# Kernel optimization log

Hardware: AMD Instinct MI355X
Metric: run time of the kernel (lower is better)

The kernel has to match this reference:

```python
import jax, jax.numpy as jnp
import numpy as np

N_NODES = 100000
N_EDGES = 1600000
D_IN = 128
D_HID = 128
LATENT = 64
N_GRAPHS = 512


def setup_inputs() -> dict:
    key = jax.random.key(0)
    ks = jax.random.split(key, 10)
    x = jax.random.normal(ks[0], (N_NODES, D_IN), dtype=jnp.float32)
    edge_index = jax.random.randint(ks[1], (2, N_EDGES), 0, N_NODES, dtype=jnp.int64)
    batch = jnp.sort(jax.random.randint(ks[2], (N_NODES,), 0, N_GRAPHS, dtype=jnp.int64))
    def lin(k, fan_in, fan_out):
        return jax.random.normal(k, (fan_in, fan_out), dtype=jnp.float32) / np.sqrt(fan_in)
    W1 = lin(ks[3], D_IN, D_HID); b1 = jnp.zeros((D_HID,), jnp.float32)
    W2 = lin(ks[4], D_HID, D_HID); b2 = jnp.zeros((D_HID,), jnp.float32)
    W3 = lin(ks[5], D_HID, 2 * LATENT); b3 = jnp.zeros((2 * LATENT,), jnp.float32)
    return {"x": x, "edge_index": edge_index, "batch": batch,
            "W1": W1, "b1": b1, "W2": W2, "b2": b2, "W3": W3, "b3": b3}


def _gcn_norm(edge_index, n_nodes):
    # PyG GCNConv default: add self-loops, symmetric normalization
    loop = jnp.arange(n_nodes, dtype=edge_index.dtype)
    src = jnp.concatenate([edge_index[0], loop])
    dst = jnp.concatenate([edge_index[1], loop])
    deg = jax.ops.segment_sum(jnp.ones_like(dst, dtype=jnp.float32), dst,
                              num_segments=n_nodes)
    dinv = jnp.where(deg > 0, jax.lax.rsqrt(deg), 0.0)
    norm = dinv[src] * dinv[dst]  # [E + N]
    return src, dst, norm


def _gcn_conv(x, W, b, src, dst, norm, n_nodes):
    h = x @ W                               # [N, d_out]
    msg = h[src] * norm[:, None]            # gather + scale, [E+N, d_out]
    agg = jax.ops.segment_sum(msg, dst, num_segments=n_nodes)
    return agg + b


def reference(x, edge_index, batch, W1, b1, W2, b2, W3, b3):
    n = x.shape[0]
    src, dst, norm = _gcn_norm(edge_index, n)
    h = jax.nn.relu(_gcn_conv(x, W1, b1, src, dst, norm, n))
    h = jax.nn.relu(_gcn_conv(h, W2, b2, src, dst, norm, n))
    h = _gcn_conv(h, W3, b3, src, dst, norm, n)
    # scatter_mean over batch ids -> [num_graphs, 2*latent]
    cnt = jax.ops.segment_sum(jnp.ones((n,), jnp.float32), batch,
                              num_segments=N_GRAPHS)
    summed = jax.ops.segment_sum(h, batch, num_segments=N_GRAPHS)
    return summed / jnp.maximum(cnt, 1.0)[:, None]
```

## Files before the change

kernel.cpp:

```cpp
#include <hip/hip_runtime.h>
#include <stdint.h>

typedef unsigned short u16;
typedef unsigned int   u32;

#define N_NODES  100000
#define N_EDGES  1600000
#define DFEAT    128
#define N_GRAPHS 512

#define NBKT   391
#define EPB    8192
#define NBLK_E 196
#define LBUF   8192

typedef float f32x4 __attribute__((ext_vector_type(4)));
typedef short s16x8 __attribute__((ext_vector_type(8)));

__device__ __forceinline__ float bflo(u32 u) { return __uint_as_float(u << 16); }
__device__ __forceinline__ float bfhi(u32 u) { return __uint_as_float(u & 0xffff0000u); }
__device__ __forceinline__ u16 f2bf(float f) {
  u32 u = __float_as_uint(f);
  return (u16)((u + 0x7fffu + ((u >> 16) & 1u)) >> 16);
}
__device__ __forceinline__ u32 pack2(float f0, float f1) {
  return (u32)f2bf(f0) | ((u32)f2bf(f1) << 16);
}

__device__ __forceinline__ int ld_src(const int* ei, int m, int e) {
  return m ? ei[2 * e] : ei[e];
}
__device__ __forceinline__ int ld_dst(const int* ei, int m, int e) {
  return m ? ei[2 * (N_EDGES + e)] : ei[N_EDGES + e];
}

__device__ __forceinline__ int detect_m_block(const int* __restrict__ ei, int* sm) {
  int t = threadIdx.x;
  if (t < 64) {
    int v = ei[2 * t + 1];
    unsigned long long b = __ballot(v != 0);
    if (t == 0) *sm = (b == 0ull) ? 1 : 0;
  }
  __syncthreads();
  return *sm;
}

__global__ __launch_bounds__(256) void histA_k(const int* __restrict__ ei,
                                               int* __restrict__ ghist,
                                               const float* __restrict__ W1,
                                               const float* __restrict__ W2,
                                               const float* __restrict__ W3,
                                               u16* __restrict__ T1, u16* __restrict__ T2,
                                               u16* __restrict__ T3, int* __restrict__ flag) {
  int t = threadIdx.x, b = blockIdx.x;
  if (b >= NBLK_E) {
    int r = b - NBLK_E;
    if (r < 3) {
      const float* W = (r == 0) ? W1 : (r == 1) ? W2 : W3;
      u16* T         = (r == 0) ? T1 : (r == 1) ? T2 : T3;
      for (int i = t; i < DFEAT * DFEAT; i += 256) {
        int n = i >> 7, k = i & 127;
        T[i] = f2bf(W[k * DFEAT + n]);
      }
    } else {
      if (t < 64) {
        int v = ei[2 * t + 1];
        unsigned long long mm = __ballot(v != 0);
        if (t == 0) *flag = (mm == 0ull) ? 1 : 0;
      }
    }
    return;
  }
  __shared__ int sm;
  __shared__ int hist[NBKT];
  int m = detect_m_block(ei, &sm);
  for (int i = t; i < NBKT; i += 256) hist[i] = 0;
  __syncthreads();
  int e0 = b * EPB;
#pragma unroll
  for (int p = 0; p < EPB / 256; p++) {
    int e = e0 + p * 256 + t;
    if (e < N_EDGES) atomicAdd(&hist[ld_dst(ei, m, e) >> 8], 1);
  }
  __syncthreads();
  for (int i = t; i < NBKT; i += 256) ghist[b * NBKT + i] = hist[i];
}

__global__ __launch_bounds__(256) void scanB1_k(int* __restrict__ ghist,
                                                int* __restrict__ gtot) {
  __shared__ int ts[256];
  int t = threadIdx.x, k = blockIdx.x;
  int v = (t < NBLK_E) ? ghist[t * NBKT + k] : 0;
  ts[t] = v;
  for (int off = 1; off < 256; off <<= 1) {
    __syncthreads(); int add = (t >= off) ? ts[t - off] : 0;
    __syncthreads(); ts[t] += add;
  }
  __syncthreads();
  if (t < NBLK_E) ghist[t * NBKT + k] = ts[t] - v;
  if (t == 255) gtot[k] = ts[255];
}

__device__ __forceinline__ void scan_gtot_block(const int* __restrict__ gtot,
                                                int* bb, int* sc) {
  int t = threadIdx.x;
  int v0 = gtot[t];
  sc[t] = v0;
  for (int off = 1; off < 256; off <<= 1) {
    __syncthreads(); int add = (t >= off) ? sc[t - off] : 0;
    __syncthreads(); sc[t] += add;
  }
  __syncthreads();
  bb[t] = sc[t] - v0;
  int base256 = sc[255];
  __syncthreads();
  int v1 = (t < NBKT - 256) ? gtot[256 + t] : 0;
  sc[t] = v1;
  for (int off = 1; off < 256; off <<= 1) {
    __syncthreads(); int add = (t >= off) ? sc[t - off] : 0;
    __syncthreads(); sc[t] += add;
  }
  __syncthreads();
  if (t < NBKT - 256) bb[256 + t] = base256 + sc[t] - v1;
  if (t == 0) bb[NBKT] = N_EDGES;
  __syncthreads();
}

__global__ __launch_bounds__(256) void scatterC_k(const int* __restrict__ ei,
                                                  const int* __restrict__ obase,
                                                  const int* __restrict__ gtot,
                                                  u32* __restrict__ colpk) {
  __shared__ int sm;
  __shared__ int cur[NBKT];
  __shared__ int bb[NBKT + 1];
  __shared__ int sc[256];
  int t = threadIdx.x, b = blockIdx.x;
  int m = detect_m_block(ei, &sm);
  scan_gtot_block(gtot, bb, sc);
  for (int i = t; i < NBKT; i += 256) cur[i] = bb[i] + obase[b * NBKT + i];
  __syncthreads();
  int e0 = b * EPB;
#pragma unroll
  for (int p = 0; p < EPB / 256; p++) {
    int e = e0 + p * 256 + t;
    if (e < N_EDGES) {
      int d = ld_dst(ei, m, e);
      int s = ld_src(ei, m, e);
      int pos = atomicAdd(&cur[d >> 8], 1);
      colpk[pos] = (u32)s | ((u32)(d & 255) << 24);
    }
  }
}

__global__ __launch_bounds__(256) void fillD_k(const int* __restrict__ gtot,
                                               const u32* __restrict__ colpk,
                                               int* __restrict__ colarr,
                                               int* __restrict__ rowptr,
                                               float* __restrict__ dinv) {
  __shared__ int hist[256];
  __shared__ int cur[256];
  __shared__ int lbuf[LBUF];
  __shared__ int bb[NBKT + 1];
  __shared__ int sc[256];
  int t = threadIdx.x, b = blockIdx.x;
  scan_gtot_block(gtot, bb, sc);
  int base = bb[b], end = bb[b + 1], cnt = end - base;
  hist[t] = 0;
  __syncthreads();
  for (int i = t; i < cnt; i += 256) atomicAdd(&hist[colpk[base + i] >> 24], 1);
  __syncthreads();
  int c = hist[t];
  cur[t] = c;
  for (int off = 1; off < 256; off <<= 1) {
    __syncthreads(); int add = (t >= off) ? cur[t - off] : 0;
    __syncthreads(); cur[t] += add;
  }
  __syncthreads();
  int excl = cur[t] - c;
  int node = b * 256 + t;
  if (node < N_NODES) {
    rowptr[node] = base + excl;
    dinv[node] = rsqrtf((float)(c + 1));
  }
  if (b == NBKT - 1 && t == 0) rowptr[N_NODES] = N_EDGES;
  __syncthreads();
  cur[t] = excl;
  __syncthreads();
  for (int i = t; i < cnt; i += 256) {
    u32 v = colpk[base + i];
    int slot = atomicAdd(&cur[v >> 24], 1);
    if (slot < LBUF) lbuf[slot] = (int)(v & 0x00FFFFFFu);
  }
  __syncthreads();
  for (int i = t; i < cnt; i += 256) colarr[base + i] = lbuf[i];
}

#define LP 136
#define GROWS 128

__global__ __launch_bounds__(512, 4) void gemm_scale_k(const void* __restrict__ Xv,
                                                       int x_is_f32,
                                                       const u16* __restrict__ Wt,
                                                       const float* __restrict__ dinv,
                                                       u16* __restrict__ Y, int nrows) {
  __shared__ u16 sW[128 * LP];
  int tid = threadIdx.x;
  int r0 = blockIdx.x * GROWS;

  for (int c = tid; c < 2048; c += 512) {
    int row = c >> 4, off = (c & 15) * 8;
    *(uint4*)(&sW[row * LP + off]) = *(const uint4*)(Wt + row * DFEAT + off);
  }
  __syncthreads();

  int wave = tid >> 6, lane = tid & 63;
  int q = lane >> 4, r = lane & 15;
  int wr0 = wave * 16;
  int arow = r0 + wr0 + r;
  bool rok = (arow < nrows);

  s16x8 a[4];
  if (x_is_f32) {
    const float* Xf = (const float*)Xv + (size_t)arow * DFEAT;
#pragma unroll
    for (int kk = 0; kk < 4; kk++) {
      uint4 u = make_uint4(0, 0, 0, 0);
      if (rok) {
        int k0 = kk * 32 + q * 8;
        float4 v0 = *(const float4*)(Xf + k0);
        float4 v1 = *(const float4*)(Xf + k0 + 4);
        u.x = pack2(v0.x, v0.y); u.y = pack2(v0.z, v0.w);
        u.z = pack2(v1.x, v1.y); u.w = pack2(v1.z, v1.w);
      }
      a[kk] = *(s16x8*)&u;
    }
  } else {
    const u16* Xb = (const u16*)Xv + (size_t)arow * DFEAT;
#pragma unroll
    for (int kk = 0; kk < 4; kk++) {
      uint4 u = make_uint4(0, 0, 0, 0);
      if (rok) u = *(const uint4*)(Xb + kk * 32 + q * 8);
      a[kk] = *(s16x8*)&u;
    }
  }

  f32x4 acc[8];
#pragma unroll
  for (int i = 0; i < 8; i++) acc[i] = (f32x4){0.f, 0.f, 0.f, 0.f};

#pragma unroll
  for (int kk = 0; kk < 4; kk++) {
    int k0 = kk * 32;
#pragma unroll
    for (int nt = 0; nt < 8; nt++) {
      s16x8 b = *(const s16x8*)(&sW[(nt * 16 + r) * LP + k0 + q * 8]);
      acc[nt] = __builtin_amdgcn_mfma_f32_16x16x32_bf16(a[kk], b, acc[nt], 0, 0, 0);
    }
  }

  __syncthreads();
#pragma unroll
  for (int i = 0; i < 4; i++) {
    int row = wr0 + q * 4 + i;
    int grow = r0 + row;
    float dv = (grow < nrows) ? dinv[grow] : 0.0f;
#pragma unroll
    for (int nt = 0; nt < 8; nt++) {
      sW[row * LP + nt * 16 + r] = f2bf(acc[nt][i] * dv);
    }
  }
  __syncthreads();
  for (int c = tid; c < 128 * 16; c += 512) {
    int row = c >> 4, seg = c & 15;
    int grow = r0 + row;
    if (grow < nrows) {
      *(uint4*)(Y + (size_t)grow * DFEAT + seg * 8) = *(const uint4*)(&sW[row * LP + seg * 8]);
    }
  }
}

struct Acc8 {
  float a0, a1, a2, a3, a4, a5, a6, a7;
  __device__ __forceinline__ void add(uint4 v) {
    a0 += bflo(v.x); a1 += bfhi(v.x); a2 += bflo(v.y); a3 += bfhi(v.y);
    a4 += bflo(v.z); a5 += bfhi(v.z); a6 += bflo(v.w); a7 += bfhi(v.w);
  }
};

#define AGG_NB_HALF 3125
#define AGG_GRID    6256

__global__ __launch_bounds__(256) void agg_k(const u32* __restrict__ HS,
                                             const float* __restrict__ dinv,
                                             const int* __restrict__ rowptr,
                                             const int* __restrict__ colidx,
                                             const float* __restrict__ bias,
                                             u32* __restrict__ OUT, int do_relu) {
  int t = threadIdx.x;
  int bid = blockIdx.x;
  int res = bid & 7;
  int half = res >> 2;
  int nb = (bid >> 3) * 4 + (res & 3);
  if (nb >= AGG_NB_HALF) return;

  int node = nb * 32 + (t >> 3);
  int fp = t & 7;
  int cbase = half * 32 + fp * 4;

  int s = rowptr[node], e = rowptr[node + 1];

  Acc8 A;
  uint4 v = *(const uint4*)(HS + (size_t)node * 64 + cbase);
  A.a0 = bflo(v.x); A.a1 = bfhi(v.x); A.a2 = bflo(v.y); A.a3 = bfhi(v.y);
  A.a4 = bflo(v.z); A.a5 = bfhi(v.z); A.a6 = bflo(v.w); A.a7 = bfhi(v.w);

  int j = s;
  for (; j + 4 <= e; j += 4) {
    int i0 = colidx[j], i1 = colidx[j + 1], i2 = colidx[j + 2], i3 = colidx[j + 3];
    uint4 w0 = *(const uint4*)(HS + (size_t)i0 * 64 + cbase);
    uint4 w1 = *(const uint4*)(HS + (size_t)i1 * 64 + cbase);
    uint4 w2 = *(const uint4*)(HS + (size_t)i2 * 64 + cbase);
    uint4 w3 = *(const uint4*)(HS + (size_t)i3 * 64 + cbase);
    A.add(w0); A.add(w1); A.add(w2); A.add(w3);
  }
  for (; j < e; j++) {
    int i0 = colidx[j];
    uint4 w0 = *(const uint4*)(HS + (size_t)i0 * 64 + cbase);
    A.add(w0);
  }

  float dv = dinv[node];
  float4 b0 = *(const float4*)(bias + cbase * 2);
  float4 b1 = *(const float4*)(bias + cbase * 2 + 4);
  float r0 = A.a0 * dv + b0.x, r1 = A.a1 * dv + b0.y;
  float r2 = A.a2 * dv + b0.z, r3 = A.a3 * dv + b0.w;
  float r4 = A.a4 * dv + b1.x, r5 = A.a5 * dv + b1.y;
  float r6 = A.a6 * dv + b1.z, r7 = A.a7 * dv + b1.w;
  if (do_relu) {
    r0 = fmaxf(r0, 0.f); r1 = fmaxf(r1, 0.f); r2 = fmaxf(r2, 0.f); r3 = fmaxf(r3, 0.f);
    r4 = fmaxf(r4, 0.f); r5 = fmaxf(r5, 0.f); r6 = fmaxf(r6, 0.f); r7 = fmaxf(r7, 0.f);
  }
  uint4 o;
  o.x = pack2(r0, r1); o.y = pack2(r2, r3); o.z = pack2(r4, r5); o.w = pack2(r6, r7);
  *(uint4*)(OUT + (size_t)node * 64 + cbase) = o;
}

__device__ __forceinline__ int lower_bound_i(const int* a, int n, int key, int shift) {
  int lo = 0, hi = n;
  while (lo < hi) {
    int mid = (lo + hi) >> 1;
    if (a[mid << shift] < key) lo = mid + 1; else hi = mid;
  }
  return lo;
}

__global__ __launch_bounds__(256) void pool_k(const u32* __restrict__ H,
                                              const int* __restrict__ batch,
                                              const int* __restrict__ flag,
                                              float* __restrict__ OUT) {
  int g = blockIdx.x;
  int m = *flag;
  int lo = lower_bound_i(batch, N_NODES, g, m);
  int hi = lower_bound_i(batch, N_NODES, g + 1, m);
  int cnt = hi - lo;
  int d2 = threadIdx.x & 63;
  int half = threadIdx.x >> 6;
  float a0 = 0.f, a1 = 0.f;
  for (int row = lo + half; row < hi; row += 4) {
    u32 v = H[(size_t)row * 64 + d2];
    a0 += bflo(v); a1 += bfhi(v);
  }
  __shared__ float red0[256], red1[256];
  red0[threadIdx.x] = a0; red1[threadIdx.x] = a1;
  __syncthreads();
  if (threadIdx.x < 64) {
    float s0 = red0[d2] + red0[d2 + 64] + red0[d2 + 128] + red0[d2 + 192];
    float s1 = red1[d2] + red1[d2 + 64] + red1[d2 + 128] + red1[d2 + 192];
    float inv = 1.0f / fmaxf((float)cnt, 1.0f);
    OUT[g * DFEAT + 2 * d2]     = s0 * inv;
    OUT[g * DFEAT + 2 * d2 + 1] = s1 * inv;
  }
}


extern "C" void kernel_launch(void* const* d_in, const int* in_sizes, int n_in,
                              void* d_out, int out_size, void* d_ws, size_t ws_size,
                              hipStream_t stream) {
  const float* x   = (const float*)d_in[0];
  const int* ei    = (const int*)d_in[1];
  const int* batch = (const int*)d_in[2];
  const float* W1  = (const float*)d_in[3];
  const float* b1  = (const float*)d_in[4];
  const float* W2  = (const float*)d_in[5];
  const float* b2  = (const float*)d_in[6];
  const float* W3  = (const float*)d_in[7];
  const float* b3  = (const float*)d_in[8];
  float* out = (float*)d_out;

  char* p = (char*)d_ws;
  size_t off = 0;
  auto carve = [&](size_t bytes) -> void* {
    void* q = p + off;
    off = (off + bytes + 255) & ~(size_t)255;
    return q;
  };
  int*   flag   = (int*)carve(256);
  int*   ghist  = (int*)carve((size_t)NBLK_E * NBKT * 4);
  int*   gtot   = (int*)carve(NBKT * 4);
  int*   rowptr = (int*)carve((N_NODES + 1) * 4);
  float* dinv   = (float*)carve(N_NODES * 4);
  u32*   colpk  = (u32*)carve((size_t)N_EDGES * 4);
  int*   colarr = (int*)carve((size_t)N_EDGES * 4);
  u16*   Wt1    = (u16*)carve(DFEAT * DFEAT * 2);
  u16*   Wt2    = (u16*)carve(DFEAT * DFEAT * 2);
  u16*   Wt3    = (u16*)carve(DFEAT * DFEAT * 2);
  u32*   bufA   = (u32*)carve((size_t)N_NODES * 64 * 4);
  u32*   bufB   = (u32*)carve((size_t)N_NODES * 64 * 4);
  (void)ws_size;

  histA_k<<<NBLK_E + 4, 256, 0, stream>>>(ei, ghist, W1, W2, W3, Wt1, Wt2, Wt3, flag);
  scanB1_k<<<NBKT, 256, 0, stream>>>(ghist, gtot);
  scatterC_k<<<NBLK_E, 256, 0, stream>>>(ei, ghist, gtot, colpk);
  fillD_k<<<NBKT, 256, 0, stream>>>(gtot, colpk, colarr, rowptr, dinv);

  const int GB = (N_NODES + GROWS - 1) / GROWS;

  gemm_scale_k<<<GB, 512, 0, stream>>>((const void*)x, 1, Wt1, dinv, (u16*)bufA, N_NODES);
  agg_k<<<AGG_GRID, 256, 0, stream>>>(bufA, dinv, rowptr, colarr, b1, bufB, 1);
  gemm_scale_k<<<GB, 512, 0, stream>>>((const void*)bufB, 0, Wt2, dinv, (u16*)bufA, N_NODES);
  agg_k<<<AGG_GRID, 256, 0, stream>>>(bufA, dinv, rowptr, colarr, b2, bufB, 1);
  gemm_scale_k<<<GB, 512, 0, stream>>>((const void*)bufB, 0, Wt3, dinv, (u16*)bufA, N_NODES);
  agg_k<<<AGG_GRID, 256, 0, stream>>>(bufA, dinv, rowptr, colarr, b3, bufB, 0);
  pool_k<<<N_GRAPHS, 256, 0, stream>>>(bufB, batch, flag, out);
}
```

Before: 383.4 us.

## Fuse first GEMM with histogram kernel; move source-degree scaling into aggregation

Moves the dinv[src] scaling out of the GEMM epilogue and into the aggregation loop, where each neighbor's dinv is gathered and applied with an FMA. With that dependency on the CSR build removed, the layer-1 GEMM no longer needs to wait for dinv, so it is merged into the first launch together with the histogram and weight-transpose blocks and overlaps the graph preprocessing. This saves one launch and hides GEMM1 behind the histogram work, but adds a scattered 4-byte dinv load per edge in each of the three aggregations.

```diff
diff --git a/kernel.cpp b/kernel.cpp
--- a/kernel.cpp
+++ b/kernel.cpp
@@ -45,20 +45,42 @@
   return *sm;
 }
 
-__global__ __launch_bounds__(256) void histA_k(const int* __restrict__ ei,
-                                               int* __restrict__ ghist,
-                                               const float* __restrict__ W1,
-                                               const float* __restrict__ W2,
-                                               const float* __restrict__ W3,
-                                               u16* __restrict__ T1, u16* __restrict__ T2,
-                                               u16* __restrict__ T3, int* __restrict__ flag) {
+#define LP 136
+#define GROWS 128
+#define GB1   782
+
+__global__ __launch_bounds__(512, 4) void fat1_k(const float* __restrict__ x,
+                                                 const float* __restrict__ W1,
+                                                 const int* __restrict__ ei,
+                                                 int* __restrict__ ghist,
+                                                 const float* __restrict__ W2,
+                                                 const float* __restrict__ W3,
+                                                 u16* __restrict__ T2, u16* __restrict__ T3,
+                                                 int* __restrict__ flag,
+                                                 u16* __restrict__ Y) {
+  __shared__ u16 sW[128 * LP];
+  __shared__ int sm;
+  __shared__ int hist[NBKT];
   int t = threadIdx.x, b = blockIdx.x;
-  if (b >= NBLK_E) {
-    int r = b - NBLK_E;
-    if (r < 3) {
-      const float* W = (r == 0) ? W1 : (r == 1) ? W2 : W3;
-      u16* T         = (r == 0) ? T1 : (r == 1) ? T2 : T3;
-      for (int i = t; i < DFEAT * DFEAT; i += 256) {
+
+  if (b >= GB1) {
+    int hb = b - GB1;
+    if (hb < NBLK_E) {
+      int m = detect_m_block(ei, &sm);
+      for (int i = t; i < NBKT; i += 512) hist[i] = 0;
+      __syncthreads();
+      int e0 = hb * EPB;
+#pragma unroll
+      for (int p = 0; p < EPB / 512; p++) {
+        int e = e0 + p * 512 + t;
+        if (e < N_EDGES) atomicAdd(&hist[ld_dst(ei, m, e) >> 8], 1);
+      }
+      __syncthreads();
+      for (int i = t; i < NBKT; i += 512) ghist[hb * NBKT + i] = hist[i];
+    } else if (hb < NBLK_E + 2) {
+      const float* W = (hb == NBLK_E) ? W2 : W3;
+      u16* T         = (hb == NBLK_E) ? T2 : T3;
+      for (int i = t; i < DFEAT * DFEAT; i += 512) {
         int n = i >> 7, k = i & 127;
         T[i] = f2bf(W[k * DFEAT + n]);
       }
@@ -71,19 +93,72 @@
     }
     return;
   }
-  __shared__ int sm;
-  __shared__ int hist[NBKT];
-  int m = detect_m_block(ei, &sm);
-  for (int i = t; i < NBKT; i += 256) hist[i] = 0;
-  __syncthreads();
-  int e0 = b * EPB;
-#pragma unroll
-  for (int p = 0; p < EPB / 256; p++) {
-    int e = e0 + p * 256 + t;
-    if (e < N_EDGES) atomicAdd(&hist[ld_dst(ei, m, e) >> 8], 1);
-  }
-  __syncthreads();
-  for (int i = t; i < NBKT; i += 256) ghist[b * NBKT + i] = hist[i];
+
+  int r0 = b * GROWS;
+  for (int c = t; c < 4096; c += 512) {
+    int k = c >> 5, n4 = (c & 31) << 2;
+    float4 v = *(const float4*)(W1 + k * DFEAT + n4);
+    sW[(n4 + 0) * LP + k] = f2bf(v.x);
+    sW[(n4 + 1) * LP + k] = f2bf(v.y);
+    sW[(n4 + 2) * LP + k] = f2bf(v.z);
+    sW[(n4 + 3) * LP + k] = f2bf(v.w);
+  }
+  __syncthreads();
+
+  int wave = t >> 6, lane = t & 63;
+  int q = lane >> 4, r = lane & 15;
+  int wr0 = wave * 16;
+  int arow = r0 + wr0 + r;
+  bool rok = (arow < N_NODES);
+
+  s16x8 a[4];
+  {
+    const float* Xf = x + (size_t)arow * DFEAT;
+#pragma unroll
+    for (int kk = 0; kk < 4; kk++) {
+      uint4 u = make_uint4(0, 0, 0, 0);
+      if (rok) {
+        int k0 = kk * 32 + q * 8;
+        float4 v0 = *(const float4*)(Xf + k0);
+        float4 v1 = *(const float4*)(Xf + k0 + 4);
+        u.x = pack2(v0.x, v0.y); u.y = pack2(v0.z, v0.w);
+        u.z = pack2(v1.x, v1.y); u.w = pack2(v1.z, v1.w);
+      }
+      a[kk] = *(s16x8*)&u;
+    }
+  }
+
+  f32x4 acc[8];
+#pragma unroll
+  for (int i = 0; i < 8; i++) acc[i] = (f32x4){0.f, 0.f, 0.f, 0.f};
+
+#pragma unroll
+  for (int kk = 0; kk < 4; kk++) {
+    int k0 = kk * 32;
+#pragma unroll
+    for (int nt = 0; nt < 8; nt++) {
+      s16x8 bb = *(const s16x8*)(&sW[(nt * 16 + r) * LP + k0 + q * 8]);
+      acc[nt] = __builtin_amdgcn_mfma_f32_16x16x32_bf16(a[kk], bb, acc[nt], 0, 0, 0);
+    }
+  }
+
+  __syncthreads();
+#pragma unroll
+  for (int i = 0; i < 4; i++) {
+    int row = wr0 + q * 4 + i;
+#pragma unroll
+    for (int nt = 0; nt < 8; nt++) {
+      sW[row * LP + nt * 16 + r] = f2bf(acc[nt][i]);
+    }
+  }
+  __syncthreads();
+  for (int c = t; c < 128 * 16; c += 512) {
+    int row = c >> 4, seg = c & 15;
+    int grow = r0 + row;
+    if (grow < N_NODES) {
+      *(uint4*)(Y + (size_t)grow * DFEAT + seg * 8) = *(const uint4*)(&sW[row * LP + seg * 8]);
+    }
+  }
 }
 
 __global__ __launch_bounds__(256) void scanB1_k(int* __restrict__ ghist,
@@ -195,14 +270,9 @@
   for (int i = t; i < cnt; i += 256) colarr[base + i] = lbuf[i];
 }
 
-#define LP 136
-#define GROWS 128
-
-__global__ __launch_bounds__(512, 4) void gemm_scale_k(const void* __restrict__ Xv,
-                                                       int x_is_f32,
-                                                       const u16* __restrict__ Wt,
-                                                       const float* __restrict__ dinv,
-                                                       u16* __restrict__ Y, int nrows) {
+__global__ __launch_bounds__(512, 4) void gemm_k(const u16* __restrict__ Xb,
+                                                 const u16* __restrict__ Wt,
+                                                 u16* __restrict__ Y, int nrows) {
   __shared__ u16 sW[128 * LP];
   int tid = threadIdx.x;
   int r0 = blockIdx.x * GROWS;
@@ -220,26 +290,12 @@
   bool rok = (arow < nrows);
 
   s16x8 a[4];
-  if (x_is_f32) {
-    const float* Xf = (const float*)Xv + (size_t)arow * DFEAT;
+  {
+    const u16* Xp = Xb + (size_t)arow * DFEAT;
 #pragma unroll
     for (int kk = 0; kk < 4; kk++) {
       uint4 u = make_uint4(0, 0, 0, 0);
-      if (rok) {
-        int k0 = kk * 32 + q * 8;
-        float4 v0 = *(const float4*)(Xf + k0);
-        float4 v1 = *(const float4*)(Xf + k0 + 4);
-        u.x = pack2(v0.x, v0.y); u.y = pack2(v0.z, v0.w);
-        u.z = pack2(v1.x, v1.y); u.w = pack2(v1.z, v1.w);
-      }
-      a[kk] = *(s16x8*)&u;
-    }
-  } else {
-    const u16* Xb = (const u16*)Xv + (size_t)arow * DFEAT;
-#pragma unroll
-    for (int kk = 0; kk < 4; kk++) {
-      uint4 u = make_uint4(0, 0, 0, 0);
-      if (rok) u = *(const uint4*)(Xb + kk * 32 + q * 8);
+      if (rok) u = *(const uint4*)(Xp + kk * 32 + q * 8);
       a[kk] = *(s16x8*)&u;
     }
   }
@@ -253,8 +309,8 @@
     int k0 = kk * 32;
 #pragma unroll
     for (int nt = 0; nt < 8; nt++) {
-      s16x8 b = *(const s16x8*)(&sW[(nt * 16 + r) * LP + k0 + q * 8]);
-      acc[nt] = __builtin_amdgcn_mfma_f32_16x16x32_bf16(a[kk], b, acc[nt], 0, 0, 0);
+      s16x8 bfrag = *(const s16x8*)(&sW[(nt * 16 + r) * LP + k0 + q * 8]);
+      acc[nt] = __builtin_amdgcn_mfma_f32_16x16x32_bf16(a[kk], bfrag, acc[nt], 0, 0, 0);
     }
   }
 
@@ -262,11 +318,9 @@
 #pragma unroll
   for (int i = 0; i < 4; i++) {
     int row = wr0 + q * 4 + i;
-    int grow = r0 + row;
-    float dv = (grow < nrows) ? dinv[grow] : 0.0f;
 #pragma unroll
     for (int nt = 0; nt < 8; nt++) {
-      sW[row * LP + nt * 16 + r] = f2bf(acc[nt][i] * dv);
+      sW[row * LP + nt * 16 + r] = f2bf(acc[nt][i]);
     }
   }
   __syncthreads();
@@ -281,9 +335,11 @@
 
 struct Acc8 {
   float a0, a1, a2, a3, a4, a5, a6, a7;
-  __device__ __forceinline__ void add(uint4 v) {
-    a0 += bflo(v.x); a1 += bfhi(v.x); a2 += bflo(v.y); a3 += bfhi(v.y);
-    a4 += bflo(v.z); a5 += bfhi(v.z); a6 += bflo(v.w); a7 += bfhi(v.w);
+  __device__ __forceinline__ void add(uint4 v, float d) {
+    a0 = fmaf(bflo(v.x), d, a0); a1 = fmaf(bfhi(v.x), d, a1);
+    a2 = fmaf(bflo(v.y), d, a2); a3 = fmaf(bfhi(v.y), d, a3);
+    a4 = fmaf(bflo(v.z), d, a4); a5 = fmaf(bfhi(v.z), d, a5);
+    a6 = fmaf(bflo(v.w), d, a6); a7 = fmaf(bfhi(v.w), d, a7);
   }
 };
 
@@ -308,34 +364,38 @@
   int cbase = half * 32 + fp * 4;
 
   int s = rowptr[node], e = rowptr[node + 1];
+  float dvs = dinv[node];
 
   Acc8 A;
   uint4 v = *(const uint4*)(HS + (size_t)node * 64 + cbase);
-  A.a0 = bflo(v.x); A.a1 = bfhi(v.x); A.a2 = bflo(v.y); A.a3 = bfhi(v.y);
-  A.a4 = bflo(v.z); A.a5 = bfhi(v.z); A.a6 = bflo(v.w); A.a7 = bfhi(v.w);
+  A.a0 = bflo(v.x) * dvs; A.a1 = bfhi(v.x) * dvs;
+  A.a2 = bflo(v.y) * dvs; A.a3 = bfhi(v.y) * dvs;
+  A.a4 = bflo(v.z) * dvs; A.a5 = bfhi(v.z) * dvs;
+  A.a6 = bflo(v.w) * dvs; A.a7 = bfhi(v.w) * dvs;
 
   int j = s;
   for (; j + 4 <= e; j += 4) {
     int i0 = colidx[j], i1 = colidx[j + 1], i2 = colidx[j + 2], i3 = colidx[j + 3];
+    float d0 = dinv[i0], d1 = dinv[i1], d2 = dinv[i2], d3 = dinv[i3];
     uint4 w0 = *(const uint4*)(HS + (size_t)i0 * 64 + cbase);
     uint4 w1 = *(const uint4*)(HS + (size_t)i1 * 64 + cbase);
     uint4 w2 = *(const uint4*)(HS + (size_t)i2 * 64 + cbase);
     uint4 w3 = *(const uint4*)(HS + (size_t)i3 * 64 + cbase);
-    A.add(w0); A.add(w1); A.add(w2); A.add(w3);
+    A.add(w0, d0); A.add(w1, d1); A.add(w2, d2); A.add(w3, d3);
   }
   for (; j < e; j++) {
     int i0 = colidx[j];
+    float d0 = dinv[i0];
     uint4 w0 = *(const uint4*)(HS + (size_t)i0 * 64 + cbase);
-    A.add(w0);
-  }
-
-  float dv = dinv[node];
+    A.add(w0, d0);
+  }
+
   float4 b0 = *(const float4*)(bias + cbase * 2);
   float4 b1 = *(const float4*)(bias + cbase * 2 + 4);
-  float r0 = A.a0 * dv + b0.x, r1 = A.a1 * dv + b0.y;
-  float r2 = A.a2 * dv + b0.z, r3 = A.a3 * dv + b0.w;
-  float r4 = A.a4 * dv + b1.x, r5 = A.a5 * dv + b1.y;
-  float r6 = A.a6 * dv + b1.z, r7 = A.a7 * dv + b1.w;
+  float r0 = A.a0 * dvs + b0.x, r1 = A.a1 * dvs + b0.y;
+  float r2 = A.a2 * dvs + b0.z, r3 = A.a3 * dvs + b0.w;
+  float r4 = A.a4 * dvs + b1.x, r5 = A.a5 * dvs + b1.y;
+  float r6 = A.a6 * dvs + b1.z, r7 = A.a7 * dvs + b1.w;
   if (do_relu) {
     r0 = fmaxf(r0, 0.f); r1 = fmaxf(r1, 0.f); r2 = fmaxf(r2, 0.f); r3 = fmaxf(r3, 0.f);
     r4 = fmaxf(r4, 0.f); r5 = fmaxf(r5, 0.f); r6 = fmaxf(r6, 0.f); r7 = fmaxf(r7, 0.f);
@@ -411,25 +471,24 @@
   float* dinv   = (float*)carve(N_NODES * 4);
   u32*   colpk  = (u32*)carve((size_t)N_EDGES * 4);
   int*   colarr = (int*)carve((size_t)N_EDGES * 4);
-  u16*   Wt1    = (u16*)carve(DFEAT * DFEAT * 2);
   u16*   Wt2    = (u16*)carve(DFEAT * DFEAT * 2);
   u16*   Wt3    = (u16*)carve(DFEAT * DFEAT * 2);
   u32*   bufA   = (u32*)carve((size_t)N_NODES * 64 * 4);
   u32*   bufB   = (u32*)carve((size_t)N_NODES * 64 * 4);
   (void)ws_size;
 
-  histA_k<<<NBLK_E + 4, 256, 0, stream>>>(ei, ghist, W1, W2, W3, Wt1, Wt2, Wt3, flag);
+  const int FAT_GRID = GB1 + NBLK_E + 3;
+
+  fat1_k<<<FAT_GRID, 512, 0, stream>>>(x, W1, ei, ghist, W2, W3, Wt2, Wt3, flag,
+                                       (u16*)bufA);
   scanB1_k<<<NBKT, 256, 0, stream>>>(ghist, gtot);
   scatterC_k<<<NBLK_E, 256, 0, stream>>>(ei, ghist, gtot, colpk);
   fillD_k<<<NBKT, 256, 0, stream>>>(gtot, colpk, colarr, rowptr, dinv);
 
-  const int GB = (N_NODES + GROWS - 1) / GROWS;
-
-  gemm_scale_k<<<GB, 512, 0, stream>>>((const void*)x, 1, Wt1, dinv, (u16*)bufA, N_NODES);
   agg_k<<<AGG_GRID, 256, 0, stream>>>(bufA, dinv, rowptr, colarr, b1, bufB, 1);
-  gemm_scale_k<<<GB, 512, 0, stream>>>((const void*)bufB, 0, Wt2, dinv, (u16*)bufA, N_NODES);
+  gemm_k<<<GB1, 512, 0, stream>>>((const u16*)bufB, Wt2, (u16*)bufA, N_NODES);
   agg_k<<<AGG_GRID, 256, 0, stream>>>(bufA, dinv, rowptr, colarr, b2, bufB, 1);
-  gemm_scale_k<<<GB, 512, 0, stream>>>((const void*)bufB, 0, Wt3, dinv, (u16*)bufA, N_NODES);
+  gemm_k<<<GB1, 512, 0, stream>>>((const u16*)bufB, Wt3, (u16*)bufA, N_NODES);
   agg_k<<<AGG_GRID, 256, 0, stream>>>(bufA, dinv, rowptr, colarr, b3, bufB, 0);
   pool_k<<<N_GRAPHS, 256, 0, stream>>>(bufB, batch, flag, out);
 }
```

After: 388.2 us. About the same (+1.3%).

## Fuse neighbor aggregation with next layer's GEMM in a single kernel

Applied to the files above, without the earlier changes.

Adds a fused kernel that, per node, gathers neighbor rows of the scaled features over the CSR adjacency. It then applies the dinv scale, bias and ReLU, and feeds the result straight into an MFMA multiply with the next layer's weights, replacing separate agg_k and gemm_scale_k launches for layers 1→2 and 2→3. This removes the write and re-read of the intermediate hidden buffer and two launches. In exchange, each thread walks one node's neighbor list serially, so per-thread gather parallelism and load balance change compared with the dedicated aggregation kernel's layout.

```diff
diff --git a/kernel.cpp b/kernel.cpp
--- a/kernel.cpp
+++ b/kernel.cpp
@@ -197,9 +197,9 @@
 
 #define LP 136
 #define GROWS 128
-
-__global__ __launch_bounds__(512, 4) void gemm_scale_k(const void* __restrict__ Xv,
-                                                       int x_is_f32,
+#define GB1   782
+
+__global__ __launch_bounds__(512, 4) void gemm_scale_k(const float* __restrict__ Xf,
                                                        const u16* __restrict__ Wt,
                                                        const float* __restrict__ dinv,
                                                        u16* __restrict__ Y, int nrows) {
@@ -220,28 +220,20 @@
   bool rok = (arow < nrows);
 
   s16x8 a[4];
-  if (x_is_f32) {
-    const float* Xf = (const float*)Xv + (size_t)arow * DFEAT;
+  {
+    const float* Xp = Xf + (size_t)arow * DFEAT;
 #pragma unroll
     for (int kk = 0; kk < 4; kk++) {
       uint4 u = make_uint4(0, 0, 0, 0);
       if (rok) {
         int k0 = kk * 32 + q * 8;
-        float4 v0 = *(const float4*)(Xf + k0);
-        float4 v1 = *(const float4*)(Xf + k0 + 4);
+        float4 v0 = *(const float4*)(Xp + k0);
+        float4 v1 = *(const float4*)(Xp + k0 + 4);
         u.x = pack2(v0.x, v0.y); u.y = pack2(v0.z, v0.w);
         u.z = pack2(v1.x, v1.y); u.w = pack2(v1.z, v1.w);
       }
       a[kk] = *(s16x8*)&u;
     }
-  } else {
-    const u16* Xb = (const u16*)Xv + (size_t)arow * DFEAT;
-#pragma unroll
-    for (int kk = 0; kk < 4; kk++) {
-      uint4 u = make_uint4(0, 0, 0, 0);
-      if (rok) u = *(const uint4*)(Xb + kk * 32 + q * 8);
-      a[kk] = *(s16x8*)&u;
-    }
   }
 
   f32x4 acc[8];
@@ -253,8 +245,8 @@
     int k0 = kk * 32;
 #pragma unroll
     for (int nt = 0; nt < 8; nt++) {
-      s16x8 b = *(const s16x8*)(&sW[(nt * 16 + r) * LP + k0 + q * 8]);
-      acc[nt] = __builtin_amdgcn_mfma_f32_16x16x32_bf16(a[kk], b, acc[nt], 0, 0, 0);
+      s16x8 bfrag = *(const s16x8*)(&sW[(nt * 16 + r) * LP + k0 + q * 8]);
+      acc[nt] = __builtin_amdgcn_mfma_f32_16x16x32_bf16(a[kk], bfrag, acc[nt], 0, 0, 0);
     }
   }
 
@@ -274,6 +266,135 @@
     int row = c >> 4, seg = c & 15;
     int grow = r0 + row;
     if (grow < nrows) {
+      *(uint4*)(Y + (size_t)grow * DFEAT + seg * 8) = *(const uint4*)(&sW[row * LP + seg * 8]);
+    }
+  }
+}
+
+__global__ __launch_bounds__(512, 4) void fusedag_k(const u32* __restrict__ HS,
+                                                    const float* __restrict__ dinv,
+                                                    const int* __restrict__ rowptr,
+                                                    const int* __restrict__ colidx,
+                                                    const float* __restrict__ bias,
+                                                    const u16* __restrict__ Wt,
+                                                    u16* __restrict__ Y) {
+  __shared__ u16 sW[128 * LP];
+  int tid = threadIdx.x;
+  int r0 = blockIdx.x * GROWS;
+
+  for (int c = tid; c < 2048; c += 512) {
+    int row = c >> 4, off = (c & 15) * 8;
+    *(uint4*)(&sW[row * LP + off]) = *(const uint4*)(Wt + row * DFEAT + off);
+  }
+  __syncthreads();
+
+  int wave = tid >> 6, lane = tid & 63;
+  int q = lane >> 4, r = lane & 15;
+  int node = r0 + wave * 16 + r;
+  int nodec = (node < N_NODES) ? node : (N_NODES - 1);
+  int q4 = q * 4;
+
+  int s = rowptr[nodec], e = rowptr[nodec + 1];
+  float dvs = dinv[nodec];
+
+  float ac[4][8];
+  {
+    const u32* pr = HS + (size_t)nodec * 64 + q4;
+#pragma unroll
+    for (int kk = 0; kk < 4; kk++) {
+      uint4 v = *(const uint4*)(pr + kk * 16);
+      ac[kk][0] = bflo(v.x); ac[kk][1] = bfhi(v.x);
+      ac[kk][2] = bflo(v.y); ac[kk][3] = bfhi(v.y);
+      ac[kk][4] = bflo(v.z); ac[kk][5] = bfhi(v.z);
+      ac[kk][6] = bflo(v.w); ac[kk][7] = bfhi(v.w);
+    }
+  }
+
+  int j = s;
+  for (; j + 2 <= e; j += 2) {
+    int i0 = colidx[j], i1 = colidx[j + 1];
+    const u32* p0 = HS + (size_t)i0 * 64 + q4;
+    const u32* p1 = HS + (size_t)i1 * 64 + q4;
+    uint4 w0[4], w1[4];
+#pragma unroll
+    for (int kk = 0; kk < 4; kk++) w0[kk] = *(const uint4*)(p0 + kk * 16);
+#pragma unroll
+    for (int kk = 0; kk < 4; kk++) w1[kk] = *(const uint4*)(p1 + kk * 16);
+#pragma unroll
+    for (int kk = 0; kk < 4; kk++) {
+      ac[kk][0] += bflo(w0[kk].x) + bflo(w1[kk].x);
+      ac[kk][1] += bfhi(w0[kk].x) + bfhi(w1[kk].x);
+      ac[kk][2] += bflo(w0[kk].y) + bflo(w1[kk].y);
+      ac[kk][3] += bfhi(w0[kk].y) + bfhi(w1[kk].y);
+      ac[kk][4] += bflo(w0[kk].z) + bflo(w1[kk].z);
+      ac[kk][5] += bfhi(w0[kk].z) + bfhi(w1[kk].z);
+      ac[kk][6] += bflo(w0[kk].w) + bflo(w1[kk].w);
+      ac[kk][7] += bfhi(w0[kk].w) + bfhi(w1[kk].w);
+    }
+  }
+  for (; j < e; j++) {
+    int i0 = colidx[j];
+    const u32* p0 = HS + (size_t)i0 * 64 + q4;
+#pragma unroll
+    for (int kk = 0; kk < 4; kk++) {
+      uint4 w = *(const uint4*)(p0 + kk * 16);
+      ac[kk][0] += bflo(w.x); ac[kk][1] += bfhi(w.x);
+      ac[kk][2] += bflo(w.y); ac[kk][3] += bfhi(w.y);
+      ac[kk][4] += bflo(w.z); ac[kk][5] += bfhi(w.z);
+      ac[kk][6] += bflo(w.w); ac[kk][7] += bfhi(w.w);
+    }
+  }
+
+  s16x8 afr[4];
+#pragma unroll
+  for (int kk = 0; kk < 4; kk++) {
+    float4 b0 = *(const float4*)(bias + kk * 32 + q * 8);
+    float4 b1v = *(const float4*)(bias + kk * 32 + q * 8 + 4);
+    float o0 = fmaxf(fmaf(ac[kk][0], dvs, b0.x), 0.f);
+    float o1 = fmaxf(fmaf(ac[kk][1], dvs, b0.y), 0.f);
+    float o2 = fmaxf(fmaf(ac[kk][2], dvs, b0.z), 0.f);
+    float o3 = fmaxf(fmaf(ac[kk][3], dvs, b0.w), 0.f);
+    float o4 = fmaxf(fmaf(ac[kk][4], dvs, b1v.x), 0.f);
+    float o5 = fmaxf(fmaf(ac[kk][5], dvs, b1v.y), 0.f);
+    float o6 = fmaxf(fmaf(ac[kk][6], dvs, b1v.z), 0.f);
+    float o7 = fmaxf(fmaf(ac[kk][7], dvs, b1v.w), 0.f);
+    uint4 u;
+    u.x = pack2(o0, o1); u.y = pack2(o2, o3);
+    u.z = pack2(o4, o5); u.w = pack2(o6, o7);
+    afr[kk] = *(s16x8*)&u;
+  }
+
+  f32x4 acc[8];
+#pragma unroll
+  for (int i = 0; i < 8; i++) acc[i] = (f32x4){0.f, 0.f, 0.f, 0.f};
+
+#pragma unroll
+  for (int kk = 0; kk < 4; kk++) {
+    int k0 = kk * 32;
+#pragma unroll
+    for (int nt = 0; nt < 8; nt++) {
+      s16x8 bfrag = *(const s16x8*)(&sW[(nt * 16 + r) * LP + k0 + q * 8]);
+      acc[nt] = __builtin_amdgcn_mfma_f32_16x16x32_bf16(afr[kk], bfrag, acc[nt], 0, 0, 0);
+    }
+  }
+
+  __syncthreads();
+  int wr0 = wave * 16;
+#pragma unroll
+  for (int i = 0; i < 4; i++) {
+    int row = wr0 + q * 4 + i;
+    int grow = r0 + row;
+    float dv = (grow < N_NODES) ? dinv[grow] : 0.0f;
+#pragma unroll
+    for (int nt = 0; nt < 8; nt++) {
+      sW[row * LP + nt * 16 + r] = f2bf(acc[nt][i] * dv);
+    }
+  }
+  __syncthreads();
+  for (int c = tid; c < 128 * 16; c += 512) {
+    int row = c >> 4, seg = c & 15;
+    int grow = r0 + row;
+    if (grow < N_NODES) {
       *(uint4*)(Y + (size_t)grow * DFEAT + seg * 8) = *(const uint4*)(&sW[row * LP + seg * 8]);
     }
   }
@@ -423,13 +544,9 @@
   scatterC_k<<<NBLK_E, 256, 0, stream>>>(ei, ghist, gtot, colpk);
   fillD_k<<<NBKT, 256, 0, stream>>>(gtot, colpk, colarr, rowptr, dinv);
 
-  const int GB = (N_NODES + GROWS - 1) / GROWS;
-
-  gemm_scale_k<<<GB, 512, 0, stream>>>((const void*)x, 1, Wt1, dinv, (u16*)bufA, N_NODES);
-  agg_k<<<AGG_GRID, 256, 0, stream>>>(bufA, dinv, rowptr, colarr, b1, bufB, 1);
-  gemm_scale_k<<<GB, 512, 0, stream>>>((const void*)bufB, 0, Wt2, dinv, (u16*)bufA, N_NODES);
-  agg_k<<<AGG_GRID, 256, 0, stream>>>(bufA, dinv, rowptr, colarr, b2, bufB, 1);
-  gemm_scale_k<<<GB, 512, 0, stream>>>((const void*)bufB, 0, Wt3, dinv, (u16*)bufA, N_NODES);
+  gemm_scale_k<<<GB1, 512, 0, stream>>>(x, Wt1, dinv, (u16*)bufA, N_NODES);
+  fusedag_k<<<GB1, 512, 0, stream>>>(bufA, dinv, rowptr, colarr, b1, Wt2, (u16*)bufB);
+  fusedag_k<<<GB1, 512, 0, stream>>>(bufB, dinv, rowptr, colarr, b2, Wt3, (u16*)bufA);
   agg_k<<<AGG_GRID, 256, 0, stream>>>(bufA, dinv, rowptr, colarr, b3, bufB, 0);
   pool_k<<<N_GRAPHS, 256, 0, stream>>>(bufB, batch, flag, out);
 }
```

Result: slower. 410.9 us (+7.2%).

## Fuse final aggregation with mean pooling via shared-memory and global atomics

Applied to the files above, without the earlier changes.

The last GCN aggregation now accumulates its per-node outputs straight into the pooled graph output. Partial sums are reduced per graph in shared memory and then added to global memory with atomics, so the separate pool kernel and the write and re-read of the final hidden buffer go away. The per-graph inverse counts and the zeroing of the output are moved into extra blocks of the scan kernel. The cost is many float atomics and a result that depends on summation order, with bf16-free fp32 accumulation of the pooled values.

```diff
diff --git a/kernel.cpp b/kernel.cpp
--- a/kernel.cpp
+++ b/kernel.cpp
@@ -43,6 +43,15 @@
   }
   __syncthreads();
   return *sm;
+}
+
+__device__ __forceinline__ int lower_bound_i(const int* a, int n, int key, int shift) {
+  int lo = 0, hi = n;
+  while (lo < hi) {
+    int mid = (lo + hi) >> 1;
+    if (a[mid << shift] < key) lo = mid + 1; else hi = mid;
+  }
+  return lo;
 }
 
 __global__ __launch_bounds__(256) void histA_k(const int* __restrict__ ei,
@@ -87,9 +96,28 @@
 }
 
 __global__ __launch_bounds__(256) void scanB1_k(int* __restrict__ ghist,
-                                                int* __restrict__ gtot) {
+                                                int* __restrict__ gtot,
+                                                const int* __restrict__ batch,
+                                                const int* __restrict__ flag,
+                                                float* __restrict__ pinv,
+                                                float* __restrict__ OUT) {
+  int t = threadIdx.x, k = blockIdx.x;
+  if (k >= NBKT) {
+    int r = k - NBKT;
+    if (r < 64) {
+      int idx = r * 1024 + t * 4;
+      *(float4*)(OUT + idx) = make_float4(0.f, 0.f, 0.f, 0.f);
+    } else {
+      int m = *flag;
+      for (int g = t; g < N_GRAPHS; g += 256) {
+        int lo = lower_bound_i(batch, N_NODES, g, m);
+        int hi = lower_bound_i(batch, N_NODES, g + 1, m);
+        pinv[g] = 1.0f / fmaxf((float)(hi - lo), 1.0f);
+      }
+    }
+    return;
+  }
   __shared__ int ts[256];
-  int t = threadIdx.x, k = blockIdx.x;
   int v = (t < NBLK_E) ? ghist[t * NBKT + k] : 0;
   ts[t] = v;
   for (int off = 1; off < 256; off <<= 1) {
@@ -197,6 +225,7 @@
 
 #define LP 136
 #define GROWS 128
+#define GB1   782
 
 __global__ __launch_bounds__(512, 4) void gemm_scale_k(const void* __restrict__ Xv,
                                                        int x_is_f32,
@@ -253,8 +282,8 @@
     int k0 = kk * 32;
 #pragma unroll
     for (int nt = 0; nt < 8; nt++) {
-      s16x8 b = *(const s16x8*)(&sW[(nt * 16 + r) * LP + k0 + q * 8]);
-      acc[nt] = __builtin_amdgcn_mfma_f32_16x16x32_bf16(a[kk], b, acc[nt], 0, 0, 0);
+      s16x8 bfrag = *(const s16x8*)(&sW[(nt * 16 + r) * LP + k0 + q * 8]);
+      acc[nt] = __builtin_amdgcn_mfma_f32_16x16x32_bf16(a[kk], bfrag, acc[nt], 0, 0, 0);
     }
   }
 
@@ -345,40 +374,95 @@
   *(uint4*)(OUT + (size_t)node * 64 + cbase) = o;
 }
 
-__device__ __forceinline__ int lower_bound_i(const int* a, int n, int key, int shift) {
-  int lo = 0, hi = n;
-  while (lo < hi) {
-    int mid = (lo + hi) >> 1;
-    if (a[mid << shift] < key) lo = mid + 1; else hi = mid;
-  }
-  return lo;
-}
-
-__global__ __launch_bounds__(256) void pool_k(const u32* __restrict__ H,
-                                              const int* __restrict__ batch,
-                                              const int* __restrict__ flag,
-                                              float* __restrict__ OUT) {
-  int g = blockIdx.x;
+__global__ __launch_bounds__(256) void agg_pool_k(const u32* __restrict__ HS,
+                                                  const float* __restrict__ dinv,
+                                                  const int* __restrict__ rowptr,
+                                                  const int* __restrict__ colidx,
+                                                  const float* __restrict__ bias,
+                                                  const int* __restrict__ batch,
+                                                  const int* __restrict__ flag,
+                                                  const float* __restrict__ pinv,
+                                                  float* __restrict__ OUT) {
+  int t = threadIdx.x;
+  int bid = blockIdx.x;
+  int res = bid & 7;
+  int half = res >> 2;
+  int nb = (bid >> 3) * 4 + (res & 3);
+  if (nb >= AGG_NB_HALF) return;
+
+  int node = nb * 32 + (t >> 3);
+  int fp = t & 7;
+  int cbase = half * 32 + fp * 4;
+
+  int s = rowptr[node], e = rowptr[node + 1];
+
+  Acc8 A;
+  uint4 v = *(const uint4*)(HS + (size_t)node * 64 + cbase);
+  A.a0 = bflo(v.x); A.a1 = bfhi(v.x); A.a2 = bflo(v.y); A.a3 = bfhi(v.y);
+  A.a4 = bflo(v.z); A.a5 = bfhi(v.z); A.a6 = bflo(v.w); A.a7 = bfhi(v.w);
+
+  int j = s;
+  for (; j + 4 <= e; j += 4) {
+    int i0 = colidx[j], i1 = colidx[j + 1], i2 = colidx[j + 2], i3 = colidx[j + 3];
+    uint4 w0 = *(const uint4*)(HS + (size_t)i0 * 64 + cbase);
+    uint4 w1 = *(const uint4*)(HS + (size_t)i1 * 64 + cbase);
+    uint4 w2 = *(const uint4*)(HS + (size_t)i2 * 64 + cbase);
+    uint4 w3 = *(const uint4*)(HS + (size_t)i3 * 64 + cbase);
+    A.add(w0); A.add(w1); A.add(w2); A.add(w3);
+  }
+  for (; j < e; j++) {
+    int i0 = colidx[j];
+    uint4 w0 = *(const uint4*)(HS + (size_t)i0 * 64 + cbase);
+    A.add(w0);
+  }
+
+  float dv = dinv[node];
+  float4 b0 = *(const float4*)(bias + cbase * 2);
+  float4 b1 = *(const float4*)(bias + cbase * 2 + 4);
+  float rv[8];
+  rv[0] = A.a0 * dv + b0.x; rv[1] = A.a1 * dv + b0.y;
+  rv[2] = A.a2 * dv + b0.z; rv[3] = A.a3 * dv + b0.w;
+  rv[4] = A.a4 * dv + b1.x; rv[5] = A.a5 * dv + b1.y;
+  rv[6] = A.a6 * dv + b1.z; rv[7] = A.a7 * dv + b1.w;
+
   int m = *flag;
-  int lo = lower_bound_i(batch, N_NODES, g, m);
-  int hi = lower_bound_i(batch, N_NODES, g + 1, m);
-  int cnt = hi - lo;
-  int d2 = threadIdx.x & 63;
-  int half = threadIdx.x >> 6;
-  float a0 = 0.f, a1 = 0.f;
-  for (int row = lo + half; row < hi; row += 4) {
-    u32 v = H[(size_t)row * 64 + d2];
-    a0 += bflo(v); a1 += bfhi(v);
-  }
-  __shared__ float red0[256], red1[256];
-  red0[threadIdx.x] = a0; red1[threadIdx.x] = a1;
-  __syncthreads();
-  if (threadIdx.x < 64) {
-    float s0 = red0[d2] + red0[d2 + 64] + red0[d2 + 128] + red0[d2 + 192];
-    float s1 = red1[d2] + red1[d2 + 64] + red1[d2 + 128] + red1[d2 + 192];
-    float inv = 1.0f / fmaxf((float)cnt, 1.0f);
-    OUT[g * DFEAT + 2 * d2]     = s0 * inv;
-    OUT[g * DFEAT + 2 * d2 + 1] = s1 * inv;
+  int g = m ? batch[2 * node] : batch[node];
+
+  __shared__ int sg0, sspan;
+  __shared__ float gacc[8][64];
+  if (t == 0) {
+    int n0 = nb * 32, n1 = nb * 32 + 31;
+    int g0 = m ? batch[2 * n0] : batch[n0];
+    int g1 = m ? batch[2 * n1] : batch[n1];
+    sg0 = g0; sspan = g1 - g0 + 1;
+  }
+  __syncthreads();
+  int g0 = sg0, span = sspan;
+
+  if (span <= 8) {
+    ((float*)gacc)[t] = 0.f;
+    ((float*)gacc)[t + 256] = 0.f;
+    __syncthreads();
+    int slot = g - g0;
+    int f0 = fp * 8;
+#pragma unroll
+    for (int i = 0; i < 8; i++) atomicAdd(&gacc[slot][f0 + i], rv[i]);
+    __syncthreads();
+    for (int sidx = t; sidx < 512; sidx += 256) {
+      int sl = sidx >> 6, f = sidx & 63;
+      if (sl < span) {
+        float val = gacc[sl][f];
+        if (val != 0.f) {
+          int gg = g0 + sl;
+          atomicAdd(&OUT[gg * DFEAT + half * 64 + f], val * pinv[gg]);
+        }
+      }
+    }
+  } else {
+    float pv = pinv[g];
+    int fbase = g * DFEAT + half * 64 + fp * 8;
+#pragma unroll
+    for (int i = 0; i < 8; i++) atomicAdd(&OUT[fbase + i], rv[i] * pv);
   }
 }
 
@@ -409,6 +493,7 @@
   int*   gtot   = (int*)carve(NBKT * 4);
   int*   rowptr = (int*)carve((N_NODES + 1) * 4);
   float* dinv   = (float*)carve(N_NODES * 4);
+  float* pinv   = (float*)carve(N_GRAPHS * 4);
   u32*   colpk  = (u32*)carve((size_t)N_EDGES * 4);
   int*   colarr = (int*)carve((size_t)N_EDGES * 4);
   u16*   Wt1    = (u16*)carve(DFEAT * DFEAT * 2);
@@ -419,17 +504,15 @@
   (void)ws_size;
 
   histA_k<<<NBLK_E + 4, 256, 0, stream>>>(ei, ghist, W1, W2, W3, Wt1, Wt2, Wt3, flag);
-  scanB1_k<<<NBKT, 256, 0, stream>>>(ghist, gtot);
+  scanB1_k<<<NBKT + 65, 256, 0, stream>>>(ghist, gtot, batch, flag, pinv, out);
   scatterC_k<<<NBLK_E, 256, 0, stream>>>(ei, ghist, gtot, colpk);
   fillD_k<<<NBKT, 256, 0, stream>>>(gtot, colpk, colarr, rowptr, dinv);
 
-  const int GB = (N_NODES + GROWS - 1) / GROWS;
-
-  gemm_scale_k<<<GB, 512, 0, stream>>>((const void*)x, 1, Wt1, dinv, (u16*)bufA, N_NODES);
+  gemm_scale_k<<<GB1, 512, 0, stream>>>((const void*)x, 1, Wt1, dinv, (u16*)bufA, N_NODES);
   agg_k<<<AGG_GRID, 256, 0, stream>>>(bufA, dinv, rowptr, colarr, b1, bufB, 1);
-  gemm_scale_k<<<GB, 512, 0, stream>>>((const void*)bufB, 0, Wt2, dinv, (u16*)bufA, N_NODES);
+  gemm_scale_k<<<GB1, 512, 0, stream>>>((const void*)bufB, 0, Wt2, dinv, (u16*)bufA, N_NODES);
   agg_k<<<AGG_GRID, 256, 0, stream>>>(bufA, dinv, rowptr, colarr, b2, bufB, 1);
-  gemm_scale_k<<<GB, 512, 0, stream>>>((const void*)bufB, 0, Wt3, dinv, (u16*)bufA, N_NODES);
-  agg_k<<<AGG_GRID, 256, 0, stream>>>(bufA, dinv, rowptr, colarr, b3, bufB, 0);
-  pool_k<<<N_GRAPHS, 256, 0, stream>>>(bufB, batch, flag, out);
-}
+  gemm_scale_k<<<GB1, 512, 0, stream>>>((const void*)bufB, 0, Wt3, dinv, (u16*)bufA, N_NODES);
+  agg_pool_k<<<AGG_GRID, 256, 0, stream>>>(bufA, dinv, rowptr, colarr, b3,
+                                           batch, flag, pinv, out);
+}
```

Measured after the change: 397.0 us. +3.6%, slower.
